# Performance work log

Measured on AMD Instinct MI355X. Metric: run time of the kernel, lower is better.

The kernel has to match this reference:

```python
import jax, jax.numpy as jnp
import numpy as np

B, C, H, W = 8, 256, 128, 128
RED = 4
LAMBDA_C = 0.5
LAMBDA_S = 0.5
EPS = 1e-5  # BatchNorm eps (eval mode: running stats)


def setup_inputs() -> dict:
    key = jax.random.key(0)
    ks = jax.random.split(key, 8)
    Cr = C // RED
    x1 = jax.random.normal(ks[0], (B, C, H, W), jnp.float32)
    x2 = jax.random.normal(ks[1], (B, C, H, W), jnp.float32)
    # feature_extractor: 1x1 conv (dim*2 -> dim), kaiming-ish scale
    w_fe = jax.random.normal(ks[2], (C, 2 * C), jnp.float32) * (2.0 / (2 * C)) ** 0.5
    bn_gamma = jnp.ones((C,), jnp.float32)
    bn_beta = jnp.zeros((C,), jnp.float32)
    bn_mean = jnp.zeros((C,), jnp.float32)
    bn_var = jnp.ones((C,), jnp.float32)
    # conv_weight_generator: C -> C//r -> 9C (1x1 convs on pooled vector)
    w_cg1 = jax.random.normal(ks[3], (Cr, C), jnp.float32) * (2.0 / C) ** 0.5
    w_cg2 = jax.random.normal(ks[4], (9 * C, Cr), jnp.float32) * (2.0 / Cr) ** 0.5
    # attention_generator: C -> C//r -> 2
    w_ag1 = jax.random.normal(ks[5], (Cr, C), jnp.float32) * (2.0 / C) ** 0.5
    w_ag2 = jax.random.normal(ks[6], (2, Cr), jnp.float32) * (2.0 / Cr) ** 0.5
    return {"x1": x1, "x2": x2, "w_fe": w_fe, "bn_gamma": bn_gamma,
            "bn_beta": bn_beta, "bn_mean": bn_mean, "bn_var": bn_var,
            "w_cg1": w_cg1, "w_cg2": w_cg2, "w_ag1": w_ag1, "w_ag2": w_ag2}


def reference(x1, x2, w_fe, bn_gamma, bn_beta, bn_mean, bn_var,
              w_cg1, w_cg2, w_ag1, w_ag2):
    Bv, Cv, Hv, Wv = x1.shape
    # feature_extractor: 1x1 conv + BN (eval) + ReLU
    cat = jnp.concatenate([x1, x2], axis=1)                       # [B,2C,H,W]
    s = jnp.einsum('oi,bihw->bohw', w_fe, cat)                    # [B,C,H,W]
    scale = (bn_gamma / jnp.sqrt(bn_var + EPS))[None, :, None, None]
    shift = (bn_beta - bn_mean * bn_gamma / jnp.sqrt(bn_var + EPS))[None, :, None, None]
    s = jax.nn.relu(s * scale + shift)
    # global average pool -> per-sample vectors
    pooled = s.mean(axis=(2, 3))                                  # [B,C]
    # dynamic per-sample, per-channel 3x3 kernels
    hcg = jax.nn.relu(pooled @ w_cg1.T)                           # [B,C//r]
    cw = (hcg @ w_cg2.T).reshape(Bv * Cv, 1, 3, 3)                # [B*C,1,3,3]
    # attention scalars (2 per sample)
    attn = jax.nn.sigmoid(jax.nn.relu(pooled @ w_ag1.T) @ w_ag2.T)  # [B,2]

    def dyn_conv(x):
        xr = x.reshape(1, Bv * Cv, Hv, Wv)
        y = jax.lax.conv_general_dilated(
            xr, cw, window_strides=(1, 1), padding='SAME',
            feature_group_count=Bv * Cv,
            dimension_numbers=('NCHW', 'OIHW', 'NCHW'))
        return y.reshape(Bv, Cv, Hv, Wv)

    d1 = dyn_conv(x1)
    d2 = dyn_conv(x2)
    a1 = attn[:, 0][:, None, None, None]
    a2 = attn[:, 1][:, None, None, None]
    out_x1 = x1 + LAMBDA_C * a1 * d1
    out_x2 = x2 + LAMBDA_C * a2 * d2
    return LAMBDA_S * out_x1 + (1.0 - LAMBDA_S) * out_x2
```

## Files before the change

### kernel.cpp

```cpp
#include <hip/hip_runtime.h>
#include <stdint.h>
#include <math.h>

#define HW_ 16384
#define C_  256
#define NT  4

typedef long i64;
typedef float f32x4 __attribute__((ext_vector_type(4)));
typedef unsigned int u32;

#define BARRIER_LGKM() asm volatile("s_waitcnt lgkmcnt(0)\n\ts_barrier" ::: "memory")

__global__ __launch_bounds__(256) void k0_prep(
    const float* __restrict__ w_fe, const float* __restrict__ gamma,
    const float* __restrict__ beta, const float* __restrict__ mean,
    const float* __restrict__ var, u32* __restrict__ Wp,
    float* __restrict__ scale, float* __restrict__ shift)
{
  int i = blockIdx.x * 256 + threadIdx.x;
  if (i < 32768) {
    int e0  = (i & 1) * 4;
    int r15 = (i >> 1) & 15;
    int kg  = (i >> 5) & 3;
    int mf  = (i >> 7) & 15;
    int ks  = i >> 11;
    int row = mf * 16 + r15;
    int k   = ks * 32 + kg * 8 + e0;
    const float* src = w_fe + row * 512 + k;
    u32 w = 0;
    w = __builtin_amdgcn_cvt_pk_fp8_f32(src[0], src[1], w, false);
    w = __builtin_amdgcn_cvt_pk_fp8_f32(src[2], src[3], w, true);
    Wp[i] = w;
  }
  if (i < 256) {
    float sc = gamma[i] * rsqrtf(var[i] + 1e-5f);
    scale[i] = sc;
    shift[i] = beta[i] - mean[i] * sc;
  }
}

__global__ __launch_bounds__(1024, 4) void k1_gemm_pool(
    const float* __restrict__ x1, const float* __restrict__ x2,
    const u32* __restrict__ Wp,
    const float* __restrict__ scale, const float* __restrict__ shift,
    float* __restrict__ pool_part)
{
  __shared__ __align__(16) char Bl[2][65536];

  const int tid  = threadIdx.x;
  const int wave = tid >> 6;
  const int lane = tid & 63;
  const int r15  = lane & 15;
  const int kg   = lane >> 4;
  const int blk  = blockIdx.x;
  const int b    = blk >> 5;
  const int t0   = (blk & 31) * NT;

  const float* xb1 = x1 + (size_t)b * C_ * HW_;
  const float* xb2 = x2 + (size_t)b * C_ * HW_;

  const int o   = tid >> 5;
  const int q   = tid & 31;
  const int pq  = q * 4;
  const int wq  = (q * 32) ^ ((o & 3) << 5);

  const int rb_off = (r15 * 8) ^ (kg << 5);

  i64 Af[16];
#pragma unroll
  for (int ks = 0; ks < 16; ++ks)
    Af[ks] = *(const i64*)((const char*)Wp
             + ((ks * 16 + wave) * 64 + kg * 16 + r15) * 8);

  const int chbase = wave * 16 + kg * 4;
  const float4 sc4 = *(const float4*)&scale[chbase];
  const float4 sh4 = *(const float4*)&shift[chbase];

  float pool0 = 0.f, pool1 = 0.f, pool2 = 0.f, pool3 = 0.f;

  f32x4 gU[4];

#define ISSUE_U(H, S, P0)                                                     \
  {                                                                           \
    const float* s0 = ((H) == 0 ? xb1 : xb2)                                  \
                      + (size_t)(o * 8 + (S) * 4) * HW_ + (P0) + pq;          \
    _Pragma("unroll")                                                         \
    for (int r = 0; r < 4; ++r) gU[r] = *(const f32x4*)(s0 + r * HW_);        \
  }

#define WRITE_U(H, S, BUF)                                                    \
  {                                                                           \
    char* wb = (char*)(BUF) + ((H) * 32 + o) * 1024 + wq + (S) * 4;           \
    _Pragma("unroll")                                                         \
    for (int j = 0; j < 4; ++j) {                                             \
      u32 w = 0;                                                              \
      w = __builtin_amdgcn_cvt_pk_fp8_f32(gU[0][j], gU[1][j], w, false);      \
      w = __builtin_amdgcn_cvt_pk_fp8_f32(gU[2][j], gU[3][j], w, true);       \
      *(u32*)(wb + j * 8) = w;                                                \
    }                                                                         \
  }

#define COMPUTE_Q(QK, BUF)                                                    \
  {                                                                           \
    _Pragma("unroll")                                                         \
    for (int ks = (QK) * 4; ks < (QK) * 4 + 4; ++ks) {                        \
      const char* rb = (const char*)(BUF) + (ks * 4 + kg) * 1024 + rb_off;    \
      _Pragma("unroll")                                                       \
      for (int nf = 0; nf < 8; ++nf) {                                        \
        i64 bq = *(const i64*)(rb + nf * 128);                                \
        acc[nf] = __builtin_amdgcn_mfma_f32_16x16x32_fp8_fp8(                 \
            Af[ks], bq, acc[nf], 0, 0, 0);                                    \
      }                                                                       \
    }                                                                         \
  }

  ISSUE_U(0, 0, t0 * 128) WRITE_U(0, 0, Bl[0])
  ISSUE_U(0, 1, t0 * 128) WRITE_U(0, 1, Bl[0])
  ISSUE_U(1, 0, t0 * 128) WRITE_U(1, 0, Bl[0])
  ISSUE_U(1, 1, t0 * 128) WRITE_U(1, 1, Bl[0])
  __syncthreads();

  for (int tt = 0; tt < NT; ++tt) {
    f32x4 acc[8];
#pragma unroll
    for (int nf = 0; nf < 8; ++nf) acc[nf] = (f32x4){0.f, 0.f, 0.f, 0.f};

    const int p1 = (t0 + tt + 1) * 128;
    const bool more = (tt + 1 < NT);
    const char* cb = Bl[tt & 1];
    char* nxt = Bl[(tt + 1) & 1];

    if (more) ISSUE_U(0, 0, p1)
    COMPUTE_Q(0, cb)
    if (more) { WRITE_U(0, 0, nxt) ISSUE_U(0, 1, p1) }
    COMPUTE_Q(1, cb)
    if (more) { WRITE_U(0, 1, nxt) ISSUE_U(1, 0, p1) }
    COMPUTE_Q(2, cb)
    if (more) { WRITE_U(1, 0, nxt) ISSUE_U(1, 1, p1) }
    COMPUTE_Q(3, cb)
    if (more) WRITE_U(1, 1, nxt)

#pragma unroll
    for (int nf = 0; nf < 8; ++nf) {
      pool0 += fmaxf(acc[nf][0] * sc4.x + sh4.x, 0.f);
      pool1 += fmaxf(acc[nf][1] * sc4.y + sh4.y, 0.f);
      pool2 += fmaxf(acc[nf][2] * sc4.z + sh4.z, 0.f);
      pool3 += fmaxf(acc[nf][3] * sc4.w + sh4.w, 0.f);
    }
    BARRIER_LGKM();
  }

#pragma unroll
  for (int m = 1; m < 16; m <<= 1) {
    pool0 += __shfl_xor(pool0, m);
    pool1 += __shfl_xor(pool1, m);
    pool2 += __shfl_xor(pool2, m);
    pool3 += __shfl_xor(pool3, m);
  }
  if (r15 == 0) {
    float* dst = pool_part + (size_t)blk * 256 + chbase;
    dst[0] = pool0; dst[1] = pool1; dst[2] = pool2; dst[3] = pool3;
  }
}

__global__ __launch_bounds__(256) void k2_small(
    const float* __restrict__ pool_part,
    const float* __restrict__ w_cg1, const float* __restrict__ w_cg2,
    const float* __restrict__ w_ag1, const float* __restrict__ w_ag2,
    float* __restrict__ cw, float* __restrict__ coef)
{
  __shared__ float pl[256];
  __shared__ float hl[64];
  const int bi = blockIdx.x;
  const int b = bi / 10, j = bi % 10;
  const int t = threadIdx.x;
  float s = 0.f;
  const float* base = pool_part + (size_t)b * 32 * 256 + t;
  for (int blk = 0; blk < 32; ++blk) s += base[blk * 256];
  pl[t] = s * (1.0f / 16384.0f);
  __syncthreads();
  if (j < 9) {
    if (t < 64) {
      float h = 0.f;
      for (int i = 0; i < 256; ++i) h += pl[i] * w_cg1[t * 256 + i];
      hl[t] = fmaxf(h, 0.f);
    }
    __syncthreads();
    const int o = t * 9 + j;
    float acc = 0.f;
    for (int jj = 0; jj < 64; ++jj) acc += hl[jj] * w_cg2[o * 64 + jj];
    cw[b * 2304 + o] = acc;
  } else {
    if (t < 64) {
      float a = 0.f;
      for (int i = 0; i < 256; ++i) a += pl[i] * w_ag1[t * 256 + i];
      hl[t] = fmaxf(a, 0.f);
    }
    __syncthreads();
    if (t < 2) {
      float acc = 0.f;
      for (int jj = 0; jj < 64; ++jj) acc += hl[jj] * w_ag2[t * 64 + jj];
      coef[b * 2 + t] = 0.25f / (1.0f + expf(-acc));
    }
  }
}

__global__ __launch_bounds__(256) void k3_dynconv(
    const float* __restrict__ x1, const float* __restrict__ x2,
    const float* __restrict__ cw, const float* __restrict__ coef,
    float* __restrict__ out)
{
  __shared__ float t1[34 * 128];
  __shared__ float t2[34 * 128];
  const int tid   = threadIdx.x;
  const int blk   = blockIdx.x;
  const int strip = blk & 3;
  const int c     = (blk >> 2) & 255;
  const int b     = blk >> 10;
  const int h0    = strip * 32;

  const size_t plane = ((size_t)b * C_ + c) * HW_;
  const float* p1 = x1 + plane;
  const float* p2 = x2 + plane;

  float tp[9];
#pragma unroll
  for (int e = 0; e < 9; ++e) tp[e] = cw[(b * C_ + c) * 9 + e];
  const float c1 = coef[b * 2 + 0];
  const float c2 = coef[b * 2 + 1];

  for (int f = tid; f < 1088; f += 256) {
    int row = f >> 5;
    int c4  = (f & 31) << 2;
    int gh  = h0 - 1 + row;
    float4 v1 = make_float4(0.f, 0.f, 0.f, 0.f), v2 = v1;
    if (gh >= 0 && gh < 128) {
      v1 = *(const float4*)&p1[gh * 128 + c4];
      v2 = *(const float4*)&p2[gh * 128 + c4];
    }
    *(float4*)&t1[row * 128 + c4] = v1;
    *(float4*)&t2[row * 128 + c4] = v2;
  }
  __syncthreads();

  for (int i = 0; i < 16; ++i) {
    int q   = tid + i * 256;
    int r   = q >> 7;
    int col = q & 127;
    int lr  = r + 1;
    const bool lok = col > 0, rok = col < 127;
    float d1 = 0.f, d2 = 0.f;
#pragma unroll
    for (int dy = 0; dy < 3; ++dy) {
      const float* row1 = &t1[(lr - 1 + dy) * 128];
      const float* row2 = &t2[(lr - 1 + dy) * 128];
      float a1v = lok ? row1[col - 1] : 0.f;
      float b1v = row1[col];
      float e1v = rok ? row1[col + 1] : 0.f;
      float a2v = lok ? row2[col - 1] : 0.f;
      float b2v = row2[col];
      float e2v = rok ? row2[col + 1] : 0.f;
      d1 += a1v * tp[dy * 3 + 0] + b1v * tp[dy * 3 + 1] + e1v * tp[dy * 3 + 2];
      d2 += a2v * tp[dy * 3 + 0] + b2v * tp[dy * 3 + 1] + e2v * tp[dy * 3 + 2];
    }
    float v1 = t1[lr * 128 + col];
    float v2 = t2[lr * 128 + col];
    out[plane + (size_t)(h0 + r) * 128 + col] = 0.5f * (v1 + v2) + c1 * d1 + c2 * d2;
  }
}

extern "C" void kernel_launch(void* const* d_in, const int* in_sizes, int n_in,
                              void* d_out, int out_size, void* d_ws, size_t ws_size,
                              hipStream_t stream) {
  const float* x1    = (const float*)d_in[0];
  const float* x2    = (const float*)d_in[1];
  const float* w_fe  = (const float*)d_in[2];
  const float* gamma = (const float*)d_in[3];
  const float* beta  = (const float*)d_in[4];
  const float* mean  = (const float*)d_in[5];
  const float* var   = (const float*)d_in[6];
  const float* w_cg1 = (const float*)d_in[7];
  const float* w_cg2 = (const float*)d_in[8];
  const float* w_ag1 = (const float*)d_in[9];
  const float* w_ag2 = (const float*)d_in[10];
  float* out = (float*)d_out;

  char* ws = (char*)d_ws;
  u32* Wp          = (u32*)(ws);
  float* scale     = (float*)(ws + 131072);
  float* shift     = (float*)(ws + 132096);
  float* pool_part = (float*)(ws + 133120);
  float* cw        = (float*)(ws + 395264);
  float* coef      = (float*)(ws + 468992);

  k0_prep<<<128, 256, 0, stream>>>(w_fe, gamma, beta, mean, var, Wp, scale, shift);
  k1_gemm_pool<<<256, 1024, 0, stream>>>(x1, x2, Wp, scale, shift, pool_part);
  k2_small<<<80, 256, 0, stream>>>(pool_part, w_cg1, w_cg2, w_ag1, w_ag2, cw, coef);
  k3_dynconv<<<8192, 256, 0, stream>>>(x1, x2, cw, coef, out);
}
```

Baseline: 152.5 us.

## Pre-quantize inputs to FP8 in separate pass before pooled GEMM

Adds a streaming kernel that converts x1 and x2 to an FP8 copy in workspace. The GEMM+pool kernel then reads 1-byte elements and only byte-shuffles them into LDS, which removes the in-loop fp32 loads and conversions. This costs an extra full read of both inputs plus a 64MB write and read, trading more total memory traffic for a lighter main kernel. The original fused path is kept as a fallback when the workspace is too small.

Result: slower. 195.5 us (+28.2%).

```diff
diff --git a/kernel.cpp b/kernel.cpp
--- a/kernel.cpp
+++ b/kernel.cpp
@@ -40,9 +40,40 @@
   }
 }
 
-__global__ __launch_bounds__(1024, 4) void k1_gemm_pool(
+__global__ __launch_bounds__(256) void kq8(
     const float* __restrict__ x1, const float* __restrict__ x2,
-    const u32* __restrict__ Wp,
+    u32* __restrict__ X8)
+{
+  const size_t g = (size_t)blockIdx.x * 256 + threadIdx.x;
+  const int R   = (int)(g >> 10);
+  const int b   = R >> 9;
+  const int r   = R & 511;
+  const int pos = (int)(g & 1023) << 4;
+  const float* src = ((r < 256) ? (x1 + ((size_t)(b * 256 + r) << 14))
+                                : (x2 + ((size_t)(b * 256 + r - 256) << 14)))
+                     + pos;
+  u32 o0, o1, o2, o3;
+  {
+    f32x4 v;
+    v = *(const f32x4*)(src);
+    o0 = __builtin_amdgcn_cvt_pk_fp8_f32(v[0], v[1], 0u, false);
+    o0 = __builtin_amdgcn_cvt_pk_fp8_f32(v[2], v[3], o0, true);
+    v = *(const f32x4*)(src + 4);
+    o1 = __builtin_amdgcn_cvt_pk_fp8_f32(v[0], v[1], 0u, false);
+    o1 = __builtin_amdgcn_cvt_pk_fp8_f32(v[2], v[3], o1, true);
+    v = *(const f32x4*)(src + 8);
+    o2 = __builtin_amdgcn_cvt_pk_fp8_f32(v[0], v[1], 0u, false);
+    o2 = __builtin_amdgcn_cvt_pk_fp8_f32(v[2], v[3], o2, true);
+    v = *(const f32x4*)(src + 12);
+    o3 = __builtin_amdgcn_cvt_pk_fp8_f32(v[0], v[1], 0u, false);
+    o3 = __builtin_amdgcn_cvt_pk_fp8_f32(v[2], v[3], o3, true);
+  }
+  u32* dst = (u32*)((char*)X8 + (((size_t)R) << 14) + pos);
+  dst[0] = o0; dst[1] = o1; dst[2] = o2; dst[3] = o3;
+}
+
+__global__ __launch_bounds__(1024, 4) void k1q(
+    const char* __restrict__ X8, const u32* __restrict__ Wp,
     const float* __restrict__ scale, const float* __restrict__ shift,
     float* __restrict__ pool_part)
 {
@@ -57,14 +88,12 @@
   const int b    = blk >> 5;
   const int t0   = (blk & 31) * NT;
 
-  const float* xb1 = x1 + (size_t)b * C_ * HW_;
-  const float* xb2 = x2 + (size_t)b * C_ * HW_;
+  const char* Xb = X8 + ((size_t)b << 23);
 
   const int o   = tid >> 5;
   const int q   = tid & 31;
   const int pq  = q * 4;
   const int wq  = (q * 32) ^ ((o & 3) << 5);
-
   const int rb_off = (r15 * 8) ^ (kg << 5);
 
   i64 Af[16];
@@ -79,14 +108,14 @@
 
   float pool0 = 0.f, pool1 = 0.f, pool2 = 0.f, pool3 = 0.f;
 
-  f32x4 gU[4];
+  u32 gq[4];
 
 #define ISSUE_U(H, S, P0)                                                     \
   {                                                                           \
-    const float* s0 = ((H) == 0 ? xb1 : xb2)                                  \
-                      + (size_t)(o * 8 + (S) * 4) * HW_ + (P0) + pq;          \
+    const char* s0 = Xb + (((size_t)((H) * 256 + o * 8 + (S) * 4)) << 14)     \
+                     + (P0) + pq;                                             \
     _Pragma("unroll")                                                         \
-    for (int r = 0; r < 4; ++r) gU[r] = *(const f32x4*)(s0 + r * HW_);        \
+    for (int r = 0; r < 4; ++r) gq[r] = *(const u32*)(s0 + ((size_t)r << 14));\
   }
 
 #define WRITE_U(H, S, BUF)                                                    \
@@ -94,9 +123,10 @@
     char* wb = (char*)(BUF) + ((H) * 32 + o) * 1024 + wq + (S) * 4;           \
     _Pragma("unroll")                                                         \
     for (int j = 0; j < 4; ++j) {                                             \
-      u32 w = 0;                                                              \
-      w = __builtin_amdgcn_cvt_pk_fp8_f32(gU[0][j], gU[1][j], w, false);      \
-      w = __builtin_amdgcn_cvt_pk_fp8_f32(gU[2][j], gU[3][j], w, true);       \
+      u32 w = ((gq[0] >> (8 * j)) & 0xffu)                                    \
+            | (((gq[1] >> (8 * j)) & 0xffu) << 8)                             \
+            | (((gq[2] >> (8 * j)) & 0xffu) << 16)                            \
+            | (((gq[3] >> (8 * j)) & 0xffu) << 24);                           \
       *(u32*)(wb + j * 8) = w;                                                \
     }                                                                         \
   }
@@ -151,6 +181,104 @@
     BARRIER_LGKM();
   }
 
+#pragma unroll
+  for (int m = 1; m < 16; m <<= 1) {
+    pool0 += __shfl_xor(pool0, m);
+    pool1 += __shfl_xor(pool1, m);
+    pool2 += __shfl_xor(pool2, m);
+    pool3 += __shfl_xor(pool3, m);
+  }
+  if (r15 == 0) {
+    float* dst = pool_part + (size_t)blk * 256 + chbase;
+    dst[0] = pool0; dst[1] = pool1; dst[2] = pool2; dst[3] = pool3;
+  }
+}
+
+__global__ __launch_bounds__(1024, 4) void k1_fb(
+    const float* __restrict__ x1, const float* __restrict__ x2,
+    const u32* __restrict__ Wp,
+    const float* __restrict__ scale, const float* __restrict__ shift,
+    float* __restrict__ pool_part)
+{
+  __shared__ __align__(16) char Bl[2][65536];
+  const int tid  = threadIdx.x;
+  const int wave = tid >> 6;
+  const int lane = tid & 63;
+  const int r15  = lane & 15;
+  const int kg   = lane >> 4;
+  const int blk  = blockIdx.x;
+  const int b    = blk >> 5;
+  const int t0   = (blk & 31) * NT;
+  const float* xb1 = x1 + (size_t)b * C_ * HW_;
+  const float* xb2 = x2 + (size_t)b * C_ * HW_;
+  const int o   = tid >> 5;
+  const int q   = tid & 31;
+  const int pq  = q * 4;
+  const int wq  = (q * 32) ^ ((o & 3) << 5);
+  const int rb_off = (r15 * 8) ^ (kg << 5);
+  i64 Af[16];
+#pragma unroll
+  for (int ks = 0; ks < 16; ++ks)
+    Af[ks] = *(const i64*)((const char*)Wp
+             + ((ks * 16 + wave) * 64 + kg * 16 + r15) * 8);
+  const int chbase = wave * 16 + kg * 4;
+  const float4 sc4 = *(const float4*)&scale[chbase];
+  const float4 sh4 = *(const float4*)&shift[chbase];
+  float pool0 = 0.f, pool1 = 0.f, pool2 = 0.f, pool3 = 0.f;
+  f32x4 gU[4];
+#define FISSUE(H, S, P0)                                                      \
+  { const float* s0 = ((H) == 0 ? xb1 : xb2)                                  \
+                      + (size_t)(o * 8 + (S) * 4) * HW_ + (P0) + pq;          \
+    _Pragma("unroll")                                                         \
+    for (int r = 0; r < 4; ++r) gU[r] = *(const f32x4*)(s0 + r * HW_); }
+#define FWRITE(H, S, BUF)                                                     \
+  { char* wb = (char*)(BUF) + ((H) * 32 + o) * 1024 + wq + (S) * 4;           \
+    _Pragma("unroll")                                                         \
+    for (int j = 0; j < 4; ++j) {                                             \
+      u32 w = 0;                                                              \
+      w = __builtin_amdgcn_cvt_pk_fp8_f32(gU[0][j], gU[1][j], w, false);      \
+      w = __builtin_amdgcn_cvt_pk_fp8_f32(gU[2][j], gU[3][j], w, true);       \
+      *(u32*)(wb + j * 8) = w; } }
+#define FCOMP(QK, BUF)                                                        \
+  { _Pragma("unroll")                                                         \
+    for (int ks = (QK) * 4; ks < (QK) * 4 + 4; ++ks) {                        \
+      const char* rb = (const char*)(BUF) + (ks * 4 + kg) * 1024 + rb_off;    \
+      _Pragma("unroll")                                                       \
+      for (int nf = 0; nf < 8; ++nf) {                                        \
+        i64 bq = *(const i64*)(rb + nf * 128);                                \
+        acc[nf] = __builtin_amdgcn_mfma_f32_16x16x32_fp8_fp8(                 \
+            Af[ks], bq, acc[nf], 0, 0, 0); } } }
+  FISSUE(0, 0, t0 * 128) FWRITE(0, 0, Bl[0])
+  FISSUE(0, 1, t0 * 128) FWRITE(0, 1, Bl[0])
+  FISSUE(1, 0, t0 * 128) FWRITE(1, 0, Bl[0])
+  FISSUE(1, 1, t0 * 128) FWRITE(1, 1, Bl[0])
+  __syncthreads();
+  for (int tt = 0; tt < NT; ++tt) {
+    f32x4 acc[8];
+#pragma unroll
+    for (int nf = 0; nf < 8; ++nf) acc[nf] = (f32x4){0.f, 0.f, 0.f, 0.f};
+    const int p1 = (t0 + tt + 1) * 128;
+    const bool more = (tt + 1 < NT);
+    const char* cb = Bl[tt & 1];
+    char* nxt = Bl[(tt + 1) & 1];
+    if (more) FISSUE(0, 0, p1)
+    FCOMP(0, cb)
+    if (more) { FWRITE(0, 0, nxt) FISSUE(0, 1, p1) }
+    FCOMP(1, cb)
+    if (more) { FWRITE(0, 1, nxt) FISSUE(1, 0, p1) }
+    FCOMP(2, cb)
+    if (more) { FWRITE(1, 0, nxt) FISSUE(1, 1, p1) }
+    FCOMP(3, cb)
+    if (more) FWRITE(1, 1, nxt)
+#pragma unroll
+    for (int nf = 0; nf < 8; ++nf) {
+      pool0 += fmaxf(acc[nf][0] * sc4.x + sh4.x, 0.f);
+      pool1 += fmaxf(acc[nf][1] * sc4.y + sh4.y, 0.f);
+      pool2 += fmaxf(acc[nf][2] * sc4.z + sh4.z, 0.f);
+      pool3 += fmaxf(acc[nf][3] * sc4.w + sh4.w, 0.f);
+    }
+    BARRIER_LGKM();
+  }
 #pragma unroll
   for (int m = 1; m < 16; m <<= 1) {
     pool0 += __shfl_xor(pool0, m);
@@ -293,9 +421,16 @@
   float* pool_part = (float*)(ws + 133120);
   float* cw        = (float*)(ws + 395264);
   float* coef      = (float*)(ws + 468992);
+  char* X8         = ws + 524288;
+  const size_t NEED = 524288 + (size_t)8 * 512 * 16384;
 
   k0_prep<<<128, 256, 0, stream>>>(w_fe, gamma, beta, mean, var, Wp, scale, shift);
-  k1_gemm_pool<<<256, 1024, 0, stream>>>(x1, x2, Wp, scale, shift, pool_part);
+  if (ws_size >= NEED) {
+    kq8<<<16384, 256, 0, stream>>>(x1, x2, (u32*)X8);
+    k1q<<<256, 1024, 0, stream>>>(X8, Wp, scale, shift, pool_part);
+  } else {
+    k1_fb<<<256, 1024, 0, stream>>>(x1, x2, Wp, scale, shift, pool_part);
+  }
   k2_small<<<80, 256, 0, stream>>>(pool_part, w_cg1, w_cg2, w_ag1, w_ag2, cw, coef);
   k3_dynconv<<<8192, 256, 0, stream>>>(x1, x2, cw, coef, out);
 }
```
